# Kernel tuning notes

Measured on AMD Instinct MI355X. Metric: run time of the kernel, lower is better.

## Reference

```python
import jax, jax.numpy as jnp
import numpy as np

B, C, D, H, W = 8, 96, 8, 32, 32
HW, DIM, NH = H * W, C * D, 4
DH = DIM // NH
EPS_NORM = 1e-12
EPS_LN = 1e-5


def setup_inputs() -> dict:
    key = jax.random.key(0)
    ks = jax.random.split(key, 10)
    s = 0.02
    return {
        "x": jax.random.normal(ks[0], (B, C, D, H, W), jnp.float32),
        "pos_embed": jax.random.normal(ks[1], (1, HW, DIM), jnp.float32) * s,
        "qkv_w": jax.random.normal(ks[2], (3 * DIM, DIM), jnp.float32) * s,
        "proj_w": jax.random.normal(ks[3], (DIM, DIM), jnp.float32) * s,
        "proj_b": jnp.zeros((DIM,), jnp.float32),
        "temperature": jnp.ones((NH, 1, 1), jnp.float32),
        "ln_gamma": jnp.ones((DIM,), jnp.float32),
        "ln_beta": jnp.zeros((DIM,), jnp.float32),
        "dw_w": jax.random.normal(ks[4], (C, 1, 3, 3, 3), jnp.float32) * s,
        "dw_b": jnp.zeros((C,), jnp.float32),
        "pw_w": jax.random.normal(ks[5], (C, C, 1, 1, 1), jnp.float32) * s,
        "pw_b": jnp.zeros((C,), jnp.float32),
    }


def _l2norm_seq(t):
    # normalize over the HW axis (dim=-2), matching F.normalize(dim=-2)
    n = jnp.sqrt(jnp.sum(t * t, axis=-2, keepdims=True))
    return t / jnp.maximum(n, EPS_NORM)


def _dsconv(y, dw_w, dw_b, pw_w, pw_b):
    dn = ("NCDHW", "OIDHW", "NCDHW")
    z = jax.lax.conv_general_dilated(y, dw_w, (1, 1, 1), [(1, 1)] * 3,
                                     dimension_numbers=dn, feature_group_count=C)
    z = z + dw_b[None, :, None, None, None]
    z = jax.lax.conv_general_dilated(z, pw_w, (1, 1, 1), [(0, 0)] * 3,
                                     dimension_numbers=dn)
    return z + pw_b[None, :, None, None, None]


def reference(x, pos_embed, qkv_w, proj_w, proj_b, temperature,
              ln_gamma, ln_beta, dw_w, dw_b, pw_w, pw_b):
    save = x
    # b c d h w -> b (h w) (c d)
    t = jnp.transpose(x, (0, 3, 4, 1, 2)).reshape(B, HW, DIM)
    t = t + pos_embed
    # qkv projection (no bias)
    qkv = (t @ qkv_w.T).reshape(B, HW, 3, NH, DH)
    qkv = jnp.transpose(qkv, (2, 0, 3, 1, 4))  # [3,B,NH,HW,DH]
    q, k, v = qkv[0], qkv[1], qkv[2]
    q = _l2norm_seq(q)
    k = _l2norm_seq(k)
    attn = jnp.einsum("bhnd,bhmd->bhnm", q, k) * temperature  # temp broadcasts [NH,1,1]
    attn = jax.nn.softmax(attn, axis=-1)  # dropout = identity at eval
    o = jnp.einsum("bhnm,bhmd->bhnd", attn, v)
    o = jnp.transpose(o, (0, 2, 1, 3)).reshape(B, HW, DIM)
    o = o @ proj_w.T + proj_b
    # LayerNorm applied to attention output
    mu = jnp.mean(o, axis=-1, keepdims=True)
    var = jnp.mean((o - mu) ** 2, axis=-1, keepdims=True)
    o = (o - mu) / jnp.sqrt(var + EPS_LN) * ln_gamma + ln_beta
    # b (h w) (c d) -> b c d h w
    o = o.reshape(B, H, W, C, D)
    o = jnp.transpose(o, (0, 3, 4, 1, 2))
    y = o + save
    return y + _dsconv(y, dw_w, dw_b, pw_w, pw_b)
```

## Files before the change

kernel.cpp:

```cpp
#include <hip/hip_runtime.h>

typedef unsigned short u16;
typedef unsigned int u32;

typedef __attribute__((ext_vector_type(8))) short short8;
typedef __attribute__((ext_vector_type(4))) float floatx4;

__device__ __forceinline__ float bf2f(u16 u) { return __uint_as_float(((u32)u) << 16); }
__device__ __forceinline__ u16 f2bf(float f) {
    u32 x = __float_as_uint(f);
    x += 0x7fffu + ((x >> 16) & 1u);
    return (u16)(x >> 16);
}
__device__ __forceinline__ void gl_lds16(const void* g, void* l) {
    __builtin_amdgcn_global_load_lds((const __attribute__((address_space(1))) u32*)g,
                                     (__attribute__((address_space(3))) u32*)l, 16, 0, 0);
}


__global__ __launch_bounds__(256) void k_init(const float* __restrict__ x,
                                              const float* __restrict__ pos,
                                              const float* __restrict__ wq,
                                              const float* __restrict__ wp,
                                              const float* __restrict__ wpw,
                                              u16* __restrict__ t,
                                              u16* __restrict__ wout,
                                              float* __restrict__ zbuf) {
    __shared__ float tile[64][65];
    const int bid = blockIdx.x;
    const int tid = threadIdx.x;
    if (bid < 1536) {
        const int cd0 = (bid % 12) * 64;
        const int hw0 = ((bid / 12) & 15) * 64;
        const int b = bid / 192;
#pragma unroll
        for (int i = 0; i < 16; i++) {
            int f = i * 256 + tid;
            int cdl = f >> 6, hwl = f & 63;
            int cd = cd0 + cdl, c = cd >> 3, d = cd & 7;
            tile[cdl][hwl] = x[(size_t)(((b * 96 + c) * 8 + d)) * 1024 + hw0 + hwl];
        }
        __syncthreads();
#pragma unroll
        for (int it = 0; it < 2; it++) {
            int u = it * 256 + tid;
            int ch = u >> 6, l = u & 63;
            int n16l = ch >> 1, kcl = ch & 1;
            int hwl = n16l * 16 + (l & 15);
            int cdl = kcl * 32 + (l >> 4) * 8;
            int row = b * 1024 + hw0 + hwl;
            int cd = cd0 + cdl;
            const float* pp = pos + (size_t)(hw0 + hwl) * 768 + cd;
            float4 p0 = *(const float4*)pp;
            float4 p1 = *(const float4*)(pp + 4);
            short8 v;
            v[0] = (short)f2bf(tile[cdl + 0][hwl] + p0.x);
            v[1] = (short)f2bf(tile[cdl + 1][hwl] + p0.y);
            v[2] = (short)f2bf(tile[cdl + 2][hwl] + p0.z);
            v[3] = (short)f2bf(tile[cdl + 3][hwl] + p0.w);
            v[4] = (short)f2bf(tile[cdl + 4][hwl] + p1.x);
            v[5] = (short)f2bf(tile[cdl + 5][hwl] + p1.y);
            v[6] = (short)f2bf(tile[cdl + 6][hwl] + p1.z);
            v[7] = (short)f2bf(tile[cdl + 7][hwl] + p1.w);
            size_t chunk = (size_t)(row >> 4) * 24 + (cd >> 5);
            *(short8*)(t + chunk * 512 + l * 8) = v;
        }
    } else if (bid < 2724) {
        const int NQ = 144 * 24 * 64;
        const int NP = NQ + 48 * 24 * 64;
        int u = (bid - 1536) * 256 + tid;
        if (u < NP) {
            const float* w = (u < NQ) ? wq : wp;
            int ub = (u < NQ) ? u : u - NQ;
            int chunk = ub >> 6, l = ub & 63;
            int n16 = chunk / 24, kc = chunk - n16 * 24;
            int n = n16 * 16 + (l & 15);
            int k0 = kc * 32 + (l >> 4) * 8;
            const float* src = w + (size_t)n * 768 + k0;
            float4 a = *(const float4*)src;
            float4 b2 = *(const float4*)(src + 4);
            short8 v;
            v[0] = (short)f2bf(a.x);  v[1] = (short)f2bf(a.y);
            v[2] = (short)f2bf(a.z);  v[3] = (short)f2bf(a.w);
            v[4] = (short)f2bf(b2.x); v[5] = (short)f2bf(b2.y);
            v[6] = (short)f2bf(b2.z); v[7] = (short)f2bf(b2.w);
            *(short8*)(wout + (size_t)u * 8) = v;
        } else {
            int i = u - NP;
            wout[(size_t)NP * 8 + i] = f2bf(wpw[i]);
        }
    } else {
        int i = (bid - 2724) * 256 + tid;
        zbuf[i] = 0.f;
    }
}

template <int MODE>
__global__ __launch_bounds__(256) void gemm_bt(const u16* __restrict__ A,
                                               const u16* __restrict__ Bw,
                                               int M, int N, int K,
                                               u16* __restrict__ qo, u16* __restrict__ ko,
                                               u16* __restrict__ vo,
                                               const float* __restrict__ bias,
                                               u16* __restrict__ Co,
                                               float* __restrict__ sqa,
                                               float* __restrict__ ska,
                                               float* __restrict__ musum,
                                               float* __restrict__ sqsum) {
    __shared__ __align__(16) u16 lAB[128 * 136];
    u16* lA = lAB;
    u16* lB = lAB + 16 * 512;
    const int tid = threadIdx.x;
    const int lane = tid & 63;
    const int wv = tid >> 6;
    const int wr = wv >> 1, wc = wv & 1;
    const int ntiles = N >> 7;
    const int mtiles = M >> 7;
    const int lin = blockIdx.x;
    const int xcd = lin & 7;
    const int idx = lin >> 3;
    const int mlocal = idx / ntiles;
    const int ntile = idx - mlocal * ntiles;
    const int m0 = (xcd * (mtiles >> 3) + mlocal) << 7;
    const int n0 = ntile << 7;
    const int lr = lane & 15;
    const int lq = lane >> 4;

    floatx4 acc[4][4];
#pragma unroll
    for (int i = 0; i < 4; i++)
#pragma unroll
        for (int j = 0; j < 4; j++) acc[i][j] = (floatx4){0.f, 0.f, 0.f, 0.f};

    const int m16 = m0 >> 4, n16 = n0 >> 4;
    for (int kc2 = 0; kc2 < (K >> 6); kc2++) {
        __syncthreads();
#pragma unroll
        for (int kh = 0; kh < 2; kh++) {
#pragma unroll
            for (int i = 0; i < 2; i++) {
                int ch16 = i * 4 + wv;
                int kc = kc2 * 2 + kh;
                const u16* ga = A + ((size_t)(m16 + ch16) * 24 + kc) * 512 + lane * 8;
                gl_lds16(ga, (char*)lA + (kh * 8 + ch16) * 1024);
                const u16* gb = Bw + ((size_t)(n16 + ch16) * 24 + kc) * 512 + lane * 8;
                gl_lds16(gb, (char*)lB + (kh * 8 + ch16) * 1024);
            }
        }
        __syncthreads();
#pragma unroll
        for (int kh = 0; kh < 2; kh++) {
            short8 af[4], bfr[4];
#pragma unroll
            for (int tt = 0; tt < 4; tt++) {
                af[tt] = *(const short8*)(lA + ((kh * 8 + wr * 4 + tt) * 64 + lane) * 8);
                bfr[tt] = *(const short8*)(lB + ((kh * 8 + wc * 4 + tt) * 64 + lane) * 8);
            }
#pragma unroll
            for (int mt = 0; mt < 4; mt++)
#pragma unroll
                for (int nt = 0; nt < 4; nt++)
                    acc[mt][nt] = __builtin_amdgcn_mfma_f32_16x16x32_bf16(af[mt], bfr[nt], acc[mt][nt], 0, 0, 0);
        }
    }

    if (MODE == 0) {
        const int region = n0 / 768;
        const int n0r = n0 - region * 768;
        const int bb0 = m0 >> 10;
        if (region < 2) {
            float* dst = (region == 0) ? sqa : ska;
#pragma unroll
            for (int nt = 0; nt < 4; nt++) {
                int colb = n0r + wc * 64 + nt * 16;
                int h = colb / 192;
                int dh = colb - h * 192 + lr;
                float s = 0.f;
#pragma unroll
                for (int mt = 0; mt < 4; mt++)
#pragma unroll
                    for (int r = 0; r < 4; r++) s += acc[mt][nt][r] * acc[mt][nt][r];
                s += __shfl_xor(s, 16);
                s += __shfl_xor(s, 32);
                if (lq == 0) atomicAdd(&dst[(bb0 * 4 + h) * 192 + dh], s);
            }
        }
        __syncthreads();
        if (region < 2) {
#pragma unroll
            for (int nt = 0; nt < 4; nt++) {
                int lch = wc * 2 + (nt >> 1);
                int offbase = (((nt & 1) * 2 + (lr >> 3)) * 16) * 8 + (lr & 7);
#pragma unroll
                for (int mt = 0; mt < 4; mt++) {
                    u16* cp2 = lAB + (((wr * 4 + mt) * 4 + lch) * 512);
#pragma unroll
                    for (int r = 0; r < 4; r++)
                        cp2[offbase + (lq * 4 + r) * 8] = f2bf(acc[mt][nt][r]);
                }
            }
        } else {
#pragma unroll
            for (int nt = 0; nt < 4; nt++) {
#pragma unroll
                for (int mt = 0; mt < 4; mt++) {
                    u16* cp2 = lAB + (((wr * 2 + (mt >> 1)) * 8 + wc * 4 + nt) * 512);
                    int ob = (((mt & 1) * 2 + (lq >> 1)) * 16 + lr) * 8 + (lq & 1) * 4;
#pragma unroll
                    for (int r = 0; r < 4; r++)
                        cp2[ob + r] = f2bf(acc[mt][nt][r]);
                }
            }
        }
        __syncthreads();
        const int b = m0 >> 10;
        const int ml = m0 & 1023;
        u16* dsto = (region == 0) ? qo : (region == 1) ? ko : vo;
#pragma unroll
        for (int i = 0; i < 8; i++) {
            int ci = wv * 8 + i;
            short8 val = *(const short8*)(lAB + ci * 512 + lane * 8);
            if (region < 2) {
                int a = ci >> 2, bb = ci & 3;
                int cg = n0r + bb * 32;
                int h = cg / 192;
                int dh32 = (cg - h * 192) >> 5;
                size_t gaddr = (size_t)(b * 4 + h) * 196608 +
                               (size_t)((((ml >> 4) + a) * 6 + dh32)) * 512 + lane * 8;
                *(short8*)(dsto + gaddr) = val;
            } else {
                int a = ci >> 3, bb = ci & 7;
                int cg = n0r + bb * 16;
                int h = cg / 192;
                int dh16 = (cg - h * 192) >> 4;
                size_t gaddr = (size_t)(b * 4 + h) * 196608 +
                               (size_t)((((ml >> 5) + a) * 12 + dh16)) * 512 + lane * 8;
                *(short8*)(dsto + gaddr) = val;
            }
        }
    } else {
        float bvv[4];
#pragma unroll
        for (int nt = 0; nt < 4; nt++) bvv[nt] = bias[n0 + wc * 64 + nt * 16 + lr];
#pragma unroll
        for (int mt = 0; mt < 4; mt++) {
#pragma unroll
            for (int r = 0; r < 4; r++) {
                float s = 0.f, ss = 0.f;
#pragma unroll
                for (int nt = 0; nt < 4; nt++) {
                    float v = acc[mt][nt][r] + bvv[nt];
                    s += v;
                    ss += v * v;
                }
#pragma unroll
                for (int m = 1; m < 16; m <<= 1) {
                    s += __shfl_xor(s, m);
                    ss += __shfl_xor(ss, m);
                }
                if (lr == 0) {
                    int row = m0 + wr * 64 + mt * 16 + lq * 4 + r;
                    atomicAdd(&musum[row], s);
                    atomicAdd(&sqsum[row], ss);
                }
            }
        }
        __syncthreads();
#pragma unroll
        for (int nt = 0; nt < 4; nt++) {
            int coll = wc * 64 + nt * 16 + lr;
#pragma unroll
            for (int mt = 0; mt < 4; mt++) {
#pragma unroll
                for (int r = 0; r < 4; r++) {
                    int rowl = wr * 64 + mt * 16 + lq * 4 + r;
                    lAB[rowl * 136 + coll] = f2bf(acc[mt][nt][r] + bvv[nt]);
                }
            }
        }
        __syncthreads();
#pragma unroll
        for (int i = 0; i < 8; i++) {
            int u = i * 256 + tid;
            int rowl = u >> 4, l = u & 15;
            short8 val = *(const short8*)(lAB + rowl * 136 + l * 8);
            *(short8*)(Co + (size_t)(m0 + rowl) * N + n0 + l * 8) = val;
        }
    }
}

__global__ __launch_bounds__(128) void k_attn(const u16* __restrict__ q,
                                              const u16* __restrict__ kmat,
                                              const u16* __restrict__ vT,
                                              const float* __restrict__ sqq,
                                              const float* __restrict__ sqk,
                                              const float* __restrict__ temp,
                                              u16* __restrict__ o) {
    __shared__ __align__(16) u16 lK[24 * 512];
    __shared__ __align__(16) u16 lV[24 * 512];
    __shared__ __align__(16) u16 lP[2 * 2048];
    __shared__ float lcs[192];
    const int lin = blockIdx.x;
    const int qb = (lin >> 3) & 15;
    const int bh = (lin & 7) * 4 + (lin >> 7);
    const int b = bh >> 2, h = bh & 3;
    const int tid = threadIdx.x;
    const int lane = tid & 63;
    const int wv = tid >> 6;
    const int lr = lane & 15;
    const int lq = lane >> 4;
    const int koff = lq * 8;

    const u16* qbase = q + (size_t)bh * 196608;
    const u16* kbase = kmat + (size_t)bh * 196608;
    const u16* vbase = vT + (size_t)bh * 196608;

    {
        const float tv = temp[bh & 3];
        for (int i = tid; i < 192; i += 128) {
            float rq = 1.f / fmaxf(sqrtf(sqq[bh * 192 + i]), 1e-12f);
            float rk = 1.f / fmaxf(sqrtf(sqk[bh * 192 + i]), 1e-12f);
            lcs[i] = rq * rk * tv;
        }
    }
    __syncthreads();

    short8 qf[2][6];
#pragma unroll
    for (int t = 0; t < 2; t++) {
        const int qr16 = qb * 4 + wv * 2 + t;
#pragma unroll
        for (int ks = 0; ks < 6; ks++) {
            short8 raw = *(const short8*)(qbase + ((size_t)(qr16 * 6 + ks)) * 512 + (size_t)lane * 8);
            short8 sc;
#pragma unroll
            for (int j = 0; j < 8; j++) {
                float f = bf2f((u16)raw[j]) * lcs[ks * 32 + koff + j];
                sc[j] = (short)f2bf(f);
            }
            qf[t][ks] = sc;
        }
    }

    float l_r[2][4];
    floatx4 oacc[2][12];
#pragma unroll
    for (int t = 0; t < 2; t++) {
#pragma unroll
        for (int r = 0; r < 4; r++) l_r[t][r] = 0.f;
#pragma unroll
        for (int vt = 0; vt < 12; vt++) oacc[t][vt] = (floatx4){0.f, 0.f, 0.f, 0.f};
    }

    u16* lp = lP + wv * 2048;

    for (int kb = 0; kb < 16; kb++) {
        __syncthreads();
#pragma unroll
        for (int i = 0; i < 12; i++) {
            int ch = i * 2 + wv;
            int ks = ch >> 2, nt = ch & 3;
            const u16* gk = kbase + ((size_t)(kb * 4 + nt) * 6 + ks) * 512 + lane * 8;
            gl_lds16(gk, (char*)lK + ch * 1024);
            int ks2 = ch / 12, vt2 = ch - ks2 * 12;
            const u16* gv = vbase + ((size_t)(kb * 2 + ks2) * 12 + vt2) * 512 + lane * 8;
            gl_lds16(gv, (char*)lV + ch * 1024);
        }
        __syncthreads();

        floatx4 s0[4], s1[4];
#pragma unroll
        for (int nt = 0; nt < 4; nt++) {
            s0[nt] = (floatx4){0.f, 0.f, 0.f, 0.f};
            s1[nt] = (floatx4){0.f, 0.f, 0.f, 0.f};
        }
        __builtin_amdgcn_s_setprio(1);
#pragma unroll
        for (int ks = 0; ks < 6; ks++) {
#pragma unroll
            for (int nt = 0; nt < 4; nt++) {
                short8 kf = *(const short8*)(lK + ((ks * 4 + nt) * 64 + lane) * 8);
                s0[nt] = __builtin_amdgcn_mfma_f32_16x16x32_bf16(qf[0][ks], kf, s0[nt], 0, 0, 0);
                s1[nt] = __builtin_amdgcn_mfma_f32_16x16x32_bf16(qf[1][ks], kf, s1[nt], 0, 0, 0);
            }
        }
        __builtin_amdgcn_s_setprio(0);

        float rs0[4] = {0.f, 0.f, 0.f, 0.f}, rs1[4] = {0.f, 0.f, 0.f, 0.f};
#pragma unroll
        for (int nt = 0; nt < 4; nt++)
#pragma unroll
            for (int r = 0; r < 4; r++) {
                float p0 = __expf(s0[nt][r]);
                s0[nt][r] = p0;
                rs0[r] += p0;
                float p1 = __expf(s1[nt][r]);
                s1[nt][r] = p1;
                rs1[r] += p1;
            }
#pragma unroll
        for (int m = 1; m < 16; m <<= 1)
#pragma unroll
            for (int r = 0; r < 4; r++) {
                rs0[r] += __shfl_xor(rs0[r], m);
                rs1[r] += __shfl_xor(rs1[r], m);
            }
#pragma unroll
        for (int r = 0; r < 4; r++) {
            l_r[0][r] += rs0[r];
            l_r[1][r] += rs1[r];
        }
#pragma unroll
        for (int nt = 0; nt < 4; nt++) {
            int base2 = (nt >> 1) * 512 + ((nt & 1) * 2 + (lr >> 3)) * 128 + (lr & 7);
#pragma unroll
            for (int r = 0; r < 4; r++) {
                lp[base2 + (lq * 4 + r) * 8] = f2bf(s0[nt][r]);
                lp[1024 + base2 + (lq * 4 + r) * 8] = f2bf(s1[nt][r]);
            }
        }

        __builtin_amdgcn_s_setprio(1);
#pragma unroll
        for (int ks2 = 0; ks2 < 2; ks2++) {
            short8 pf0 = *(const short8*)(lp + ks2 * 512 + lane * 8);
            short8 pf1 = *(const short8*)(lp + 1024 + ks2 * 512 + lane * 8);
#pragma unroll
            for (int vt = 0; vt < 12; vt++) {
                short8 vf = *(const short8*)(lV + ((ks2 * 12 + vt) * 64 + lane) * 8);
                oacc[0][vt] = __builtin_amdgcn_mfma_f32_16x16x32_bf16(pf0, vf, oacc[0][vt], 0, 0, 0);
                oacc[1][vt] = __builtin_amdgcn_mfma_f32_16x16x32_bf16(pf1, vf, oacc[1][vt], 0, 0, 0);
            }
        }
        __builtin_amdgcn_s_setprio(0);
    }

    __syncthreads();
#pragma unroll
    for (int t = 0; t < 2; t++) {
        float inv[4];
#pragma unroll
        for (int r = 0; r < 4; r++) inv[r] = 1.f / l_r[t][r];
#pragma unroll
        for (int vt = 0; vt < 12; vt++) {
            int col = vt * 16 + lr;
            int swb = (col >> 5) * 512 + (((col >> 3) & 3) * 16) * 8 + (col & 7);
#pragma unroll
            for (int r = 0; r < 4; r++) {
                int rowl = wv * 32 + t * 16 + lq * 4 + r;
                lK[(rowl >> 4) * 3072 + swb + (rowl & 15) * 8] = f2bf(oacc[t][vt][r] * inv[r]);
            }
        }
    }
    __syncthreads();
#pragma unroll
    for (int i = 0; i < 12; i++) {
        int u = i * 128 + tid;
        int chl = u >> 6, l = u & 63;
        short8 val = *(const short8*)(lK + chl * 512 + l * 8);
        int a = chl / 6, kc = chl - a * 6;
        size_t gaddr = ((size_t)(b * 64 + qb * 4 + a) * 24 + h * 6 + kc) * 512 + l * 8;
        *(short8*)(o + gaddr) = val;
    }
}

__global__ __launch_bounds__(256) void k_lnt(const u16* __restrict__ o2,
                                             const float* __restrict__ musum,
                                             const float* __restrict__ sqsum,
                                             const float* __restrict__ gamma,
                                             const float* __restrict__ beta,
                                             const float* __restrict__ x,
                                             float* __restrict__ y) {
    __shared__ float tile[64][65];
    const int b = blockIdx.z, hw0 = blockIdx.y * 64, cd0 = blockIdx.x * 64;
    const int tid = threadIdx.x;
#pragma unroll
    for (int i = 0; i < 16; i++) {
        int f = i * 256 + tid;
        int hwl = f >> 6, cdl = f & 63;
        int row = b * 1024 + hw0 + hwl;
        float m_ = musum[row] * (1.f / 768.f);
        float var = fmaxf(sqsum[row] * (1.f / 768.f) - m_ * m_, 0.f);
        float rstd = rsqrtf(var + 1e-5f);
        float v = bf2f(o2[(size_t)row * 768 + cd0 + cdl]);
        v = (v - m_) * rstd * gamma[cd0 + cdl] + beta[cd0 + cdl];
        tile[hwl][cdl] = v;
    }
    __syncthreads();
#pragma unroll
    for (int i = 0; i < 16; i++) {
        int f = i * 256 + tid;
        int cdl = f >> 6, hwl = f & 63;
        int cd = cd0 + cdl, c = cd >> 3, d = cd & 7;
        size_t addr = (size_t)((b * 96 + c) * 8 + d) * 1024 + hw0 + hwl;
        y[addr] = tile[hwl][cdl] + x[addr];
    }
}

__global__ __launch_bounds__(256) void k_dw(const float* __restrict__ y,
                                            const float* __restrict__ w,
                                            const float* __restrict__ bias,
                                            u16* __restrict__ z) {
    __shared__ float ly[8192];
    const int bc = blockIdx.x;
    const int c = bc % 96;
    const int tid = threadIdx.x;
    const size_t base = (size_t)bc * 8192;

#pragma unroll
    for (int i = 0; i < 8; i++) {
        int i4 = i * 256 + tid;
        *(float4*)(ly + i4 * 4) = *(const float4*)(y + base + i4 * 4);
    }
    float wt[27];
#pragma unroll
    for (int j = 0; j < 27; j++) wt[j] = w[c * 27 + j];
    const float bv = bias[c];
    __syncthreads();

    const int wcol = tid & 31;
    const int hh = tid >> 5;

    for (int hb = 0; hb < 4; hb++) {
        const int h = hb * 8 + hh;
        float pl[3][9];
        auto loadplane = [&](int dd, float* p) {
#pragma unroll
            for (int kh = 0; kh < 3; kh++) {
                int h2 = h + kh - 1;
                bool hok = (unsigned)h2 < 32u;
                const float* row = ly + dd * 1024 + h2 * 32;
#pragma unroll
                for (int kw = 0; kw < 3; kw++) {
                    int w2 = wcol + kw - 1;
                    bool ok = hok && (unsigned)w2 < 32u;
                    p[kh * 3 + kw] = ok ? row[w2] : 0.f;
                }
            }
        };
#pragma unroll
        for (int j = 0; j < 9; j++) pl[0][j] = 0.f;
        loadplane(0, pl[1]);
#pragma unroll
        for (int d = 0; d < 8; d++) {
            if (d < 7) loadplane(d + 1, pl[2]);
            else {
#pragma unroll
                for (int j = 0; j < 9; j++) pl[2][j] = 0.f;
            }
            float acc = bv;
#pragma unroll
            for (int kd = 0; kd < 3; kd++)
#pragma unroll
                for (int j = 0; j < 9; j++) acc += wt[kd * 9 + j] * pl[kd][j];
            z[base + d * 1024 + h * 32 + wcol] = f2bf(acc);
#pragma unroll
            for (int j = 0; j < 9; j++) { pl[0][j] = pl[1][j]; pl[1][j] = pl[2][j]; }
        }
    }
}

__global__ __launch_bounds__(256) void k_pw(const u16* __restrict__ z,
                                            const u16* __restrict__ wbf,
                                            const float* __restrict__ bias,
                                            float* __restrict__ out) {
    __shared__ __align__(16) u16 lZ[128 * 104];
    __shared__ __align__(16) u16 lW[96 * 104];
    const int tid = threadIdx.x;
    const int lane = tid & 63;
    const int wv = tid >> 6;
    const int lr = lane & 15;
    const int lq = lane >> 4;
    const int koff = lq * 8;

    const int idx = blockIdx.x;
    const int q = idx & 7;
    const int bd = idx >> 3;
    const int b = bd >> 3, d = bd & 7;
    const int pos0 = q * 128;

    for (int i = tid; i < 96 * 96; i += 256) {
        int row = i / 96, col = i - row * 96;
        lW[row * 104 + col] = wbf[i];
    }
    {
        const int pos = tid & 127;
        const int cc0 = (tid >> 7) * 48;
        const size_t gbase = ((size_t)b * 96 * 8 + d) * 1024 + pos0 + pos;
#pragma unroll
        for (int g = 0; g < 6; g++) {
            short8 v;
#pragma unroll
            for (int j = 0; j < 8; j++) {
                int cc = cc0 + g * 8 + j;
                v[j] = (short)z[gbase + (size_t)cc * 8192];
            }
            *(short8*)(lZ + pos * 104 + cc0 + g * 8) = v;
        }
    }
    __syncthreads();

    floatx4 acc[6][2];
#pragma unroll
    for (int m = 0; m < 6; m++)
#pragma unroll
        for (int nt = 0; nt < 2; nt++) acc[m][nt] = (floatx4){0.f, 0.f, 0.f, 0.f};

#pragma unroll
    for (int ks = 0; ks < 3; ks++) {
        short8 bfrg[2];
#pragma unroll
        for (int nt = 0; nt < 2; nt++)
            bfrg[nt] = *(const short8*)(lZ + (wv * 32 + nt * 16 + lr) * 104 + ks * 32 + koff);
#pragma unroll
        for (int m = 0; m < 6; m++) {
            short8 afr = *(const short8*)(lW + (m * 16 + lr) * 104 + ks * 32 + koff);
#pragma unroll
            for (int nt = 0; nt < 2; nt++)
                acc[m][nt] = __builtin_amdgcn_mfma_f32_16x16x32_bf16(afr, bfrg[nt], acc[m][nt], 0, 0, 0);
        }
    }

#pragma unroll
    for (int m = 0; m < 6; m++) {
#pragma unroll
        for (int r = 0; r < 4; r++) {
            int c = m * 16 + lq * 4 + r;
            float bv = bias[c];
            size_t rowbase = ((size_t)(b * 96 + c) * 8 + d) * 1024 + pos0;
#pragma unroll
            for (int nt = 0; nt < 2; nt++) {
                int pos = wv * 32 + nt * 16 + lr;
                size_t a = rowbase + pos;
                out[a] = out[a] + bv + acc[m][nt][r];
            }
        }
    }
}

extern "C" void kernel_launch(void* const* d_in, const int* in_sizes, int n_in,
                              void* d_out, int out_size, void* d_ws, size_t ws_size,
                              hipStream_t stream) {
    (void)in_sizes; (void)n_in; (void)out_size; (void)ws_size;
    const float* x      = (const float*)d_in[0];
    const float* pos    = (const float*)d_in[1];
    const float* qkv_w  = (const float*)d_in[2];
    const float* proj_w = (const float*)d_in[3];
    const float* proj_b = (const float*)d_in[4];
    const float* temp   = (const float*)d_in[5];
    const float* ln_g   = (const float*)d_in[6];
    const float* ln_b   = (const float*)d_in[7];
    const float* dw_w   = (const float*)d_in[8];
    const float* dw_b   = (const float*)d_in[9];
    const float* pw_w   = (const float*)d_in[10];
    const float* pw_b   = (const float*)d_in[11];
    float* out = (float*)d_out;
    char* ws = (char*)d_ws;

    u16* t    = (u16*)(ws + 0);
    u16* vT   = (u16*)(ws + 12582912);
    u16* q    = (u16*)(ws + 25165824);
    u16* kk   = (u16*)(ws + 37748736);
    u16* wqb  = (u16*)(ws + 50331648);
    float* sqq   = (float*)(ws + 55175168);
    float* sqk   = (float*)(ws + 55199744);
    float* musum = (float*)(ws + 55224320);
    float* sqsum = (float*)(ws + 55257088);
    u16* wpb  = wqb + 2304 * 768;
    u16* wpwb = wqb + 2304 * 768 + 768 * 768;
    u16* o   = t;
    u16* o2  = q;
    u16* z   = t;
    float* y  = out;

    k_init<<<2836, 256, 0, stream>>>(x, pos, qkv_w, proj_w, pw_w, t, wqb, sqq);
    gemm_bt<0><<<1152, 256, 0, stream>>>(t, wqb, 8192, 2304, 768, q, kk, vT, nullptr, nullptr,
                                         sqq, sqk, nullptr, nullptr);
    k_attn<<<512, 128, 0, stream>>>(q, kk, vT, sqq, sqk, temp, o);
    gemm_bt<1><<<384, 256, 0, stream>>>(o, wpb, 8192, 768, 768, nullptr, nullptr, nullptr, proj_b,
                                        o2, nullptr, nullptr, musum, sqsum);
    k_lnt<<<dim3(12, 16, 8), 256, 0, stream>>>(o2, musum, sqsum, ln_g, ln_b, x, y);
    k_dw<<<768, 256, 0, stream>>>(y, dw_w, dw_b, z);
    k_pw<<<512, 256, 0, stream>>>(z, wpwb, pw_b, out);
}
```

Measured before the change: 259.2 us.

## Overlap next K/V tile loads with softmax and PV compute in attention loop

Splits the per-block K and V global-to-LDS staging into separate phases and issues the next block's K load right after QK^T and the next V load right after PV. Manual vmcnt waits and raw s_barrier calls replace the two __syncthreads per iteration. The goal is to hide global load latency behind exp/rowsum and MFMA work. The risk is that raw barriers with vmcnt accounting are fragile. The last stage_V is followed by a wait on vmcnt(12), which appears to leave the 12 just-issued V loads outstanding before the next iteration's QK^T, and the K-side waits are similarly loose.

New measurement: 261.1 us. About the same (+0.7%).

```diff
diff --git a/kernel.cpp b/kernel.cpp
--- a/kernel.cpp
+++ b/kernel.cpp
@@ -354,20 +354,32 @@
 
     u16* lp = lP + wv * 2048;
 
-    for (int kb = 0; kb < 16; kb++) {
-        __syncthreads();
+    auto stage_K = [&](int kb2) {
 #pragma unroll
         for (int i = 0; i < 12; i++) {
             int ch = i * 2 + wv;
             int ks = ch >> 2, nt = ch & 3;
-            const u16* gk = kbase + ((size_t)(kb * 4 + nt) * 6 + ks) * 512 + lane * 8;
+            const u16* gk = kbase + ((size_t)(kb2 * 4 + nt) * 6 + ks) * 512 + lane * 8;
             gl_lds16(gk, (char*)lK + ch * 1024);
+        }
+    };
+    auto stage_V = [&](int kb2) {
+#pragma unroll
+        for (int i = 0; i < 12; i++) {
+            int ch = i * 2 + wv;
             int ks2 = ch / 12, vt2 = ch - ks2 * 12;
-            const u16* gv = vbase + ((size_t)(kb * 2 + ks2) * 12 + vt2) * 512 + lane * 8;
+            const u16* gv = vbase + ((size_t)(kb2 * 2 + ks2) * 12 + vt2) * 512 + lane * 8;
             gl_lds16(gv, (char*)lV + ch * 1024);
         }
-        __syncthreads();
-
+    };
+
+    asm volatile("s_waitcnt vmcnt(0)" ::: "memory");
+    stage_K(0);
+    stage_V(0);
+    asm volatile("s_waitcnt vmcnt(12)" ::: "memory");
+    __builtin_amdgcn_s_barrier();
+
+    for (int kb = 0; kb < 16; kb++) {
         floatx4 s0[4], s1[4];
 #pragma unroll
         for (int nt = 0; nt < 4; nt++) {
@@ -385,6 +397,8 @@
             }
         }
         __builtin_amdgcn_s_setprio(0);
+        __builtin_amdgcn_s_barrier();
+        if (kb < 15) stage_K(kb + 1);
 
         float rs0[4] = {0.f, 0.f, 0.f, 0.f}, rs1[4] = {0.f, 0.f, 0.f, 0.f};
 #pragma unroll
@@ -420,6 +434,10 @@
             }
         }
 
+        if (kb < 15) { asm volatile("s_waitcnt vmcnt(12)" ::: "memory"); }
+        else         { asm volatile("s_waitcnt vmcnt(0)" ::: "memory"); }
+        __builtin_amdgcn_s_barrier();
+
         __builtin_amdgcn_s_setprio(1);
 #pragma unroll
         for (int ks2 = 0; ks2 < 2; ks2++) {
@@ -433,6 +451,12 @@
             }
         }
         __builtin_amdgcn_s_setprio(0);
+        __builtin_amdgcn_s_barrier();
+        if (kb < 15) {
+            stage_V(kb + 1);
+            asm volatile("s_waitcnt vmcnt(12)" ::: "memory");
+            __builtin_amdgcn_s_barrier();
+        }
     }
 
     __syncthreads();
```
